# Kernel optimization log

Measured on AMD Instinct MI355X. Metric: run time of the kernel, lower is better.

The kernel has to match this reference:

```python
import jax, jax.numpy as jnp
import numpy as np

CHAINS = [[15, 14, 13], [10, 11, 12], [5, 4, 3], [0, 1, 2]]
B, H, I = 2048, 1024, 3


def setup_inputs() -> dict:
    key = jax.random.key(0)
    ks = jax.random.split(key, 8)
    s = 1.0 / np.sqrt(H)
    return {
        "p3d": jax.random.normal(ks[0], (B, 16, I), dtype=jnp.float32),
        "Wih": jax.random.uniform(ks[1], (4 * H, I), jnp.float32, -s, s),
        "Whh": jax.random.uniform(ks[2], (4 * H, H), jnp.float32, -s, s),
        "bih": jax.random.uniform(ks[3], (4 * H,), jnp.float32, -s, s),
        "bhh": jax.random.uniform(ks[4], (4 * H,), jnp.float32, -s, s),
        "Wref": jax.random.uniform(ks[5], (I, H), jnp.float32, -s, s),
        "bref": jax.random.uniform(ks[6], (I,), jnp.float32, -s, s),
    }


def reference(p3d, Wih, Whh, bih, bhh, Wref, bref):
    # p3d: [B, 16, 3]; shared LSTMCell traverses the skeleton tree fwd+back.
    def cell(x, h, c):
        gates = x @ Wih.T + bih + h @ Whh.T + bhh  # [B, 4H]
        i, f, g, o = jnp.split(gates, 4, axis=-1)  # torch gate order i,f,g,o
        c2 = jax.nn.sigmoid(f) * c + jax.nn.sigmoid(i) * jnp.tanh(g)
        return jax.nn.sigmoid(o) * jnp.tanh(c2), c2

    z = jnp.zeros((p3d.shape[0], Whh.shape[1]), p3d.dtype)
    fh, fc = {}, {}
    # forward pass along limb chains (root of each chain starts from zeros)
    for chain in CHAINS:
        h, c = cell(p3d[:, chain[0]], z, z)
        fh[chain[0]], fc[chain[0]] = h, c
        for prev, cur in zip(chain[:-1], chain[1:]):
            h, c = cell(p3d[:, cur], fh[prev], fc[prev])
            fh[cur], fc[cur] = h, c
    # spine: merge hip ends (joints 2, 3) -> 6 -> 7
    hx, cx = (fh[2] + fh[3]) / 2, (fc[2] + fc[3]) / 2
    fh[6], fc[6] = cell(p3d[:, 6], hx, cx)
    fh[7], fc[7] = cell(p3d[:, 7], fh[6], fc[6])
    # merge neck + wrist ends (joints 7, 13, 12) -> 8 -> 9
    hx = (fh[7] + fh[13] + fh[12]) / 3
    cx = (fc[7] + fc[13] + fc[12]) / 3
    fh[8], fc[8] = cell(p3d[:, 8], hx, cx)
    fh[9], fc[9] = cell(p3d[:, 9], fh[8], fc[8])

    bh, bc = {}, {}
    bh[9], bc[9] = cell(p3d[:, 9], z, z)
    hx, cx = bh[9], bc[9]
    for i in [8, 7, 6]:
        hx, cx = cell(p3d[:, i], hx, cx)
        bh[i], bc[i] = hx, cx
    for chain in CHAINS:
        if chain[2] > 9:
            hx, cx = bh[8], bc[8]
        else:
            hx, cx = bh[6], bc[6]
        for i in reversed(chain):
            hx, cx = cell(p3d[:, i], hx, cx)
            bh[i], bc[i] = hx, cx

    FH = jnp.stack([fh[j] for j in range(16)], axis=1)  # [B, 16, H]
    BH = jnp.stack([bh[j] for j in range(16)], axis=1)  # [B, 16, H]
    out = (FH + BH) / 2.0
    return out @ Wref.T + bref  # [B, 16, 3]
```

## Files before the change

### kernel.cpp

```cpp
#include <hip/hip_runtime.h>
#include <cmath>

#define Bsz 2048
#define Hsz 1024
#define NG  4096
#define BM  128
#define BK  32
#define NKT 32
#define NBUF 3

typedef __attribute__((ext_vector_type(8))) short bf16x8;
typedef __attribute__((ext_vector_type(4))) float f32x4;

struct CellArgs {
  int ncells, b0;
  int joint[8];
  const short* hih[8];
  const short* hil[8];
  const float* cin[8];
  short* hoh[8];
  short* hol[8];
  float* cout[8];
};

struct ProjArgs {
  int ncells, b0;
  int joint[8];
  const short* hh[8];
  const short* hl[8];
};

__device__ __forceinline__ float sigmoidf_(float x) {
  return 1.0f / (1.0f + __expf(-x));
}
__device__ __forceinline__ float fast_tanh(float x) {
  float ax = fabsf(x);
  float e = __expf(2.0f * ax);
  float t = 1.0f - 2.0f / (e + 1.0f);
  return copysignf(t, x);
}
__device__ __forceinline__ float bf2f(short b) {
  unsigned u = ((unsigned)(unsigned short)b) << 16;
  float f; __builtin_memcpy(&f, &u, 4); return f;
}
__device__ __forceinline__ short f2bf(float f) {
  unsigned u; __builtin_memcpy(&u, &f, 4);
  u += 0x7fffu + ((u >> 16) & 1u);
  return (short)(u >> 16);
}
__device__ __forceinline__ void gl_lds16(const void* g, void* l) {
  __builtin_amdgcn_global_load_lds(
      (const __attribute__((address_space(1))) unsigned int*)g,
      (__attribute__((address_space(3))) unsigned int*)l, 16, 0, 0);
}
template <int N> __device__ __forceinline__ void vmw() {
  asm volatile("s_waitcnt vmcnt(%0)" :: "n"(N) : "memory");
}
__device__ __forceinline__ void lgkm0() {
  asm volatile("s_waitcnt lgkmcnt(0)" ::: "memory");
  __builtin_amdgcn_sched_barrier(0);
}

__launch_bounds__(256, 3)
__global__ void cell_kernel(const float* __restrict__ p3d,
                            const short* __restrict__ Whi,
                            const float4* __restrict__ wb,
                            CellArgs A) {
  __shared__ short Atile[NBUF][BM * BK];
  __shared__ short Btile[NBUF][BM * BK];
  __shared__ float xs[BM * 4];

  const int z = blockIdx.z;
  const short* __restrict__ hih = A.hih[z];
  const float* __restrict__ cin = A.cin[z];
  short* __restrict__ hoh = A.hoh[z];
  short* __restrict__ hol = A.hol[z];
  float* __restrict__ co  = A.cout[z];

  const int t = threadIdx.x;
  const int lane = t & 63;
  const int w = t >> 6;
  const int wm = w >> 1;
  const int wn = w & 1;
  const int m0 = blockIdx.x * BM;
  const int hc0 = blockIdx.y * 32;
  const int lc = lane & 15;
  const int kg = lane >> 4;

  const int l2 = lane >> 2;
  const int sslot = ((((lane & 3) - ((lane >> 3) & 3)) & 3) * 8);
  int aOff[2], bOff[2];
  #pragma unroll
  for (int j = 0; j < 2; ++j) {
    const int chunk = j * 4 + w;
    aOff[j] = (m0 + chunk * 16 + l2) * Hsz + sslot;
    const int np = chunk * 16 + l2;
    const int g = np >> 5;
    const int hcl = np & 31;
    bOff[j] = (g * Hsz + hc0 + hcl) * Hsz + sslot;
  }

  if (t < BM) {
    const float* p = p3d + ((size_t)(A.b0 + m0 + t) * 16 + A.joint[z]) * 3;
    xs[t * 4 + 0] = p[0];
    xs[t * 4 + 1] = p[1];
    xs[t * 4 + 2] = p[2];
  }
  __syncthreads();

  f32x4 acc[4][4];
  #pragma unroll
  for (int mf = 0; mf < 4; ++mf)
    #pragma unroll
    for (int nf = 0; nf < 4; ++nf) acc[mf][nf] = (f32x4){0.f, 0.f, 0.f, 0.f};

  const bool hasH = (hih != nullptr);

  auto stage = [&](int kt, int buf) {
    const int k0 = kt * BK;
    #pragma unroll
    for (int j = 0; j < 2; ++j)
      gl_lds16(hih + aOff[j] + k0, &Atile[buf][(j * 4 + w) * 512]);
    #pragma unroll
    for (int j = 0; j < 2; ++j)
      gl_lds16(Whi + bOff[j] + k0, &Btile[buf][(j * 4 + w) * 512]);
  };

  if (hasH) {
    const int rslot = ((kg + (lc >> 1)) & 3) * 8;
    const int aRB = (wm * 64 + lc) * BK + rslot;
    const int bRB = (wn * 16 + lc) * BK + rslot;

    stage(0, 0);
    stage(1, 1);
    vmw<4>();
    __builtin_amdgcn_s_barrier();

    int rb = 0;
    for (int kt = 0; kt < NKT; ++kt) {
      const int sb = (rb + 2 >= NBUF) ? rb + 2 - NBUF : rb + 2;
      if (kt + 2 < NKT) stage(kt + 2, sb);
      const short* Ab = &Atile[rb][0];
      const short* Bb = &Btile[rb][0];
      bf16x8 af[4], bf[4];
      #pragma unroll
      for (int mf = 0; mf < 4; ++mf)
        af[mf] = *(const bf16x8*)(Ab + aRB + mf * 512);
      #pragma unroll
      for (int nf = 0; nf < 4; ++nf)
        bf[nf] = *(const bf16x8*)(Bb + bRB + nf * 1024);
      lgkm0();
      __builtin_amdgcn_s_setprio(1);
      #pragma unroll
      for (int mf = 0; mf < 4; ++mf)
        #pragma unroll
        for (int nf = 0; nf < 4; ++nf)
          acc[mf][nf] = __builtin_amdgcn_mfma_f32_16x16x32_bf16(
              af[mf], bf[nf], acc[mf][nf], 0, 0, 0);
      __builtin_amdgcn_s_setprio(0);
      if (kt + 2 < NKT) vmw<4>();
      else vmw<0>();
      __builtin_amdgcn_s_barrier();
      rb = (rb + 1 >= NBUF) ? 0 : rb + 1;
    }
  }

  const int hc = hc0 + wn * 16 + lc;
  float4 wv[4];
  #pragma unroll
  for (int g = 0; g < 4; ++g) wv[g] = wb[g * Hsz + hc];
  #pragma unroll
  for (int mf = 0; mf < 4; ++mf) {
    #pragma unroll
    for (int r = 0; r < 4; ++r) {
      const int ml = wm * 64 + mf * 16 + kg * 4 + r;
      const int m = m0 + ml;
      const float x0 = xs[ml * 4 + 0], x1 = xs[ml * 4 + 1], x2 = xs[ml * 4 + 2];
      float pre[4];
      #pragma unroll
      for (int g = 0; g < 4; ++g)
        pre[g] = acc[mf][g][r] + wv[g].w + x0 * wv[g].x + x1 * wv[g].y + x2 * wv[g].z;
      const float ci = cin ? cin[(size_t)m * Hsz + hc] : 0.0f;
      const float c2 = sigmoidf_(pre[1]) * ci + sigmoidf_(pre[0]) * fast_tanh(pre[2]);
      const float h2 = sigmoidf_(pre[3]) * fast_tanh(c2);
      co[(size_t)m * Hsz + hc] = c2;
      const short hhi = f2bf(h2);
      hoh[(size_t)m * Hsz + hc] = hhi;
      hol[(size_t)m * Hsz + hc] = f2bf(h2 - bf2f(hhi));
    }
  }
}

__global__ void prep_kernel(const float* __restrict__ Whh,
                            const float* __restrict__ Wih,
                            const float* __restrict__ bih,
                            const float* __restrict__ bhh,
                            short* __restrict__ Whi,
                            float4* __restrict__ wb) {
  const int n4 = NG * Hsz / 4;
  int i = blockIdx.x * blockDim.x + threadIdx.x;
  for (; i < n4; i += gridDim.x * blockDim.x) {
    float4 wv = reinterpret_cast<const float4*>(Whh)[i];
    short4 hi;
    hi.x = f2bf(wv.x);
    hi.y = f2bf(wv.y);
    hi.z = f2bf(wv.z);
    hi.w = f2bf(wv.w);
    reinterpret_cast<short4*>(Whi)[i] = hi;
  }
  int c = blockIdx.x * blockDim.x + threadIdx.x;
  if (c < NG)
    wb[c] = make_float4(Wih[c * 3], Wih[c * 3 + 1], Wih[c * 3 + 2],
                        bih[c] + bhh[c]);
}

__global__ void merge_kernel(short* __restrict__ ohh, short* __restrict__ ohl,
                             float* __restrict__ oc,
                             const short* __restrict__ ahh, const short* __restrict__ ahl,
                             const float* __restrict__ ac,
                             const short* __restrict__ bhh, const short* __restrict__ bhl,
                             const float* __restrict__ bc,
                             const short* __restrict__ chh, const short* __restrict__ chl,
                             const float* __restrict__ cc,
                             float scale, int n4) {
  int i = blockIdx.x * blockDim.x + threadIdx.x;
  for (; i < n4; i += gridDim.x * blockDim.x) {
    short4 ah = reinterpret_cast<const short4*>(ahh)[i];
    short4 al = reinterpret_cast<const short4*>(ahl)[i];
    short4 bh = reinterpret_cast<const short4*>(bhh)[i];
    short4 bl = reinterpret_cast<const short4*>(bhl)[i];
    float h[4];
    h[0] = bf2f(ah.x) + bf2f(al.x) + bf2f(bh.x) + bf2f(bl.x);
    h[1] = bf2f(ah.y) + bf2f(al.y) + bf2f(bh.y) + bf2f(bl.y);
    h[2] = bf2f(ah.z) + bf2f(al.z) + bf2f(bh.z) + bf2f(bl.z);
    h[3] = bf2f(ah.w) + bf2f(al.w) + bf2f(bh.w) + bf2f(bl.w);
    float4 c = reinterpret_cast<const float4*>(ac)[i];
    float4 c2 = reinterpret_cast<const float4*>(bc)[i];
    c.x += c2.x; c.y += c2.y; c.z += c2.z; c.w += c2.w;
    if (chh != nullptr) {
      short4 ch = reinterpret_cast<const short4*>(chh)[i];
      short4 cl = reinterpret_cast<const short4*>(chl)[i];
      h[0] += bf2f(ch.x) + bf2f(cl.x);
      h[1] += bf2f(ch.y) + bf2f(cl.y);
      h[2] += bf2f(ch.z) + bf2f(cl.z);
      h[3] += bf2f(ch.w) + bf2f(cl.w);
      float4 c3 = reinterpret_cast<const float4*>(cc)[i];
      c.x += c3.x; c.y += c3.y; c.z += c3.z; c.w += c3.w;
    }
    short4 hi, lo;
    float v;
    v = h[0] * scale; hi.x = f2bf(v); lo.x = f2bf(v - bf2f(hi.x));
    v = h[1] * scale; hi.y = f2bf(v); lo.y = f2bf(v - bf2f(hi.y));
    v = h[2] * scale; hi.z = f2bf(v); lo.z = f2bf(v - bf2f(hi.z));
    v = h[3] * scale; hi.w = f2bf(v); lo.w = f2bf(v - bf2f(hi.w));
    reinterpret_cast<short4*>(ohh)[i] = hi;
    reinterpret_cast<short4*>(ohl)[i] = lo;
    c.x *= scale; c.y *= scale; c.z *= scale; c.w *= scale;
    reinterpret_cast<float4*>(oc)[i] = c;
  }
}

__global__ void init_out_kernel(float* __restrict__ out, const float* __restrict__ bref) {
  int i = blockIdx.x * blockDim.x + threadIdx.x;
  const int n = Bsz * 16 * 3;
  for (; i < n; i += gridDim.x * blockDim.x) out[i] = bref[i % 3];
}

__global__ void proj_kernel(ProjArgs P, const float* __restrict__ Wref,
                            float* __restrict__ out) {
  const int cell = blockIdx.x;
  const int b = blockIdx.y;
  const int t = threadIdx.x;
  const short4* hh = reinterpret_cast<const short4*>(P.hh[cell] + (size_t)b * Hsz);
  const short4* hl = reinterpret_cast<const short4*>(P.hl[cell] + (size_t)b * Hsz);
  const float4* W0 = reinterpret_cast<const float4*>(Wref);
  const float4* W1 = reinterpret_cast<const float4*>(Wref + Hsz);
  const float4* W2 = reinterpret_cast<const float4*>(Wref + 2 * Hsz);
  short4 a = hh[t], l = hl[t];
  float v0 = 0.5f * (bf2f(a.x) + bf2f(l.x));
  float v1 = 0.5f * (bf2f(a.y) + bf2f(l.y));
  float v2 = 0.5f * (bf2f(a.z) + bf2f(l.z));
  float v3 = 0.5f * (bf2f(a.w) + bf2f(l.w));
  float4 w0 = W0[t], w1 = W1[t], w2 = W2[t];
  float s0 = v0 * w0.x + v1 * w0.y + v2 * w0.z + v3 * w0.w;
  float s1 = v0 * w1.x + v1 * w1.y + v2 * w1.z + v3 * w1.w;
  float s2 = v0 * w2.x + v1 * w2.y + v2 * w2.z + v3 * w2.w;
  #pragma unroll
  for (int off = 32; off > 0; off >>= 1) {
    s0 += __shfl_down(s0, off);
    s1 += __shfl_down(s1, off);
    s2 += __shfl_down(s2, off);
  }
  __shared__ float red[4][3];
  const int wave = t >> 6;
  if ((t & 63) == 0) { red[wave][0] = s0; red[wave][1] = s1; red[wave][2] = s2; }
  __syncthreads();
  if (t == 0) {
    float r0 = red[0][0] + red[1][0] + red[2][0] + red[3][0];
    float r1 = red[0][1] + red[1][1] + red[2][1] + red[3][1];
    float r2 = red[0][2] + red[1][2] + red[2][2] + red[3][2];
    float* o = out + ((size_t)(P.b0 + b) * 16 + P.joint[cell]) * 3;
    atomicAdd(o + 0, r0);
    atomicAdd(o + 1, r1);
    atomicAdd(o + 2, r2);
  }
}

extern "C" void kernel_launch(void* const* d_in, const int* in_sizes, int n_in,
                              void* d_out, int out_size, void* d_ws, size_t ws_size,
                              hipStream_t stream) {
  const float* p3d  = (const float*)d_in[0];
  const float* Wih  = (const float*)d_in[1];
  const float* Whh  = (const float*)d_in[2];
  const float* bih  = (const float*)d_in[3];
  const float* bhh  = (const float*)d_in[4];
  const float* Wref = (const float*)d_in[5];
  const float* bref = (const float*)d_in[6];
  float* out = (float*)d_out;

  char* ws = (char*)d_ws;
  short* Whi = (short*)ws;
  float4* wb = (float4*)(Whi + (size_t)NG * Hsz);
  char* pool = (char*)(wb + NG);
  const size_t fixed = (size_t)(pool - ws);

  int chunkB = Bsz;
  while (chunkB > BM && fixed + (size_t)12 * chunkB * Hsz * 8 > ws_size)
    chunkB >>= 1;
  const size_t CH = (size_t)chunkB * Hsz;
  auto SH = [&](int s) { return (short*)(pool + (size_t)s * CH * 8); };
  auto SL = [&](int s) { return SH(s) + CH; };
  auto SC = [&](int s) { return (float*)(SL(s) + CH); };

  const dim3 blk(256);
  prep_kernel<<<dim3(4096), blk, 0, stream>>>(Whh, Wih, bih, bhh, Whi, wb);
  init_out_kernel<<<dim3(96), blk, 0, stream>>>(out, bref);

  for (int b0 = 0; b0 < Bsz; b0 += chunkB) {
    auto run_cells = [&](CellArgs& A) {
      A.b0 = b0;
      dim3 grid(chunkB / BM, Hsz / 32, A.ncells);
      cell_kernel<<<grid, blk, 0, stream>>>(p3d, Whi, wb, A);
    };
    auto run_proj = [&](ProjArgs& P) {
      P.b0 = b0;
      proj_kernel<<<dim3(P.ncells, chunkB), blk, 0, stream>>>(P, Wref, out);
    };
    auto cellset = [&](CellArgs& A, int i, int joint, int sin, int sout) {
      A.joint[i] = joint;
      if (sin >= 0) { A.hih[i] = SH(sin); A.hil[i] = SL(sin); A.cin[i] = SC(sin); }
      else          { A.hih[i] = nullptr; A.hil[i] = nullptr; A.cin[i] = nullptr; }
      A.hoh[i] = SH(sout); A.hol[i] = SL(sout); A.cout[i] = SC(sout);
    };
    auto projset = [&](ProjArgs& P, int i, int joint, int s) {
      P.joint[i] = joint; P.hh[i] = SH(s); P.hl[i] = SL(s);
    };
    auto domerge = [&](int dst, int s1, int s2, int s3, float scale) {
      merge_kernel<<<dim3(1024), blk, 0, stream>>>(
          SH(dst), SL(dst), SC(dst), SH(s1), SL(s1), SC(s1),
          SH(s2), SL(s2), SC(s2),
          s3 >= 0 ? SH(s3) : nullptr, s3 >= 0 ? SL(s3) : nullptr,
          s3 >= 0 ? SC(s3) : nullptr, scale, (int)(CH / 4));
    };

    {
      CellArgs A{}; A.ncells = 5;
      cellset(A, 0, 15, -1, 0); cellset(A, 1, 10, -1, 1); cellset(A, 2, 5, -1, 2);
      cellset(A, 3,  0, -1, 3); cellset(A, 4,  9, -1, 4);
      run_cells(A);
      ProjArgs P{}; P.ncells = 5;
      projset(P, 0, 15, 0); projset(P, 1, 10, 1); projset(P, 2, 5, 2);
      projset(P, 3,  0, 3); projset(P, 4,  9, 4);
      run_proj(P);
    }
    {
      CellArgs A{}; A.ncells = 5;
      cellset(A, 0, 14, 0, 5); cellset(A, 1, 11, 1, 6); cellset(A, 2, 4, 2, 7);
      cellset(A, 3,  1, 3, 8); cellset(A, 4,  8, 4, 9);
      run_cells(A);
      ProjArgs P{}; P.ncells = 5;
      projset(P, 0, 14, 5); projset(P, 1, 11, 6); projset(P, 2, 4, 7);
      projset(P, 3,  1, 8); projset(P, 4,  8, 9);
      run_proj(P);
    }
    {
      CellArgs A{}; A.ncells = 7;
      cellset(A, 0, 13, 5, 0);  cellset(A, 1, 12, 6, 1);  cellset(A, 2, 3, 7, 2);
      cellset(A, 3,  2, 8, 3);  cellset(A, 4,  7, 9, 4);  cellset(A, 5, 13, 9, 10);
      cellset(A, 6, 12, 9, 11);
      run_cells(A);
      ProjArgs P{}; P.ncells = 7;
      projset(P, 0, 13, 0);  projset(P, 1, 12, 1);  projset(P, 2, 3, 2);
      projset(P, 3,  2, 3);  projset(P, 4,  7, 4);  projset(P, 5, 13, 10);
      projset(P, 6, 12, 11);
      run_proj(P);
    }
    domerge(5, 3, 2, -1, 0.5f);
    {
      CellArgs A{}; A.ncells = 4;
      cellset(A, 0,  6, 5, 6);  cellset(A, 1,  6, 4, 7);
      cellset(A, 2, 14, 10, 8); cellset(A, 3, 11, 11, 9);
      run_cells(A);
      ProjArgs P{}; P.ncells = 4;
      projset(P, 0, 6, 6); projset(P, 1, 6, 7); projset(P, 2, 14, 8);
      projset(P, 3, 11, 9);
      run_proj(P);
    }
    {
      CellArgs A{}; A.ncells = 5;
      cellset(A, 0,  7, 6, 4);  cellset(A, 1, 15, 8, 5);  cellset(A, 2, 10, 9, 10);
      cellset(A, 3,  3, 7, 11); cellset(A, 4,  2, 7, 2);
      run_cells(A);
      ProjArgs P{}; P.ncells = 5;
      projset(P, 0, 7, 4);  projset(P, 1, 15, 5); projset(P, 2, 10, 10);
      projset(P, 3, 3, 11); projset(P, 4,  2, 2);
      run_proj(P);
    }
    domerge(6, 4, 0, 1, 1.0f / 3.0f);
    {
      CellArgs A{}; A.ncells = 3;
      cellset(A, 0, 8, 6, 0); cellset(A, 1, 4, 11, 1); cellset(A, 2, 1, 2, 3);
      run_cells(A);
      ProjArgs P{}; P.ncells = 3;
      projset(P, 0, 8, 0); projset(P, 1, 4, 1); projset(P, 2, 1, 3);
      run_proj(P);
    }
    {
      CellArgs A{}; A.ncells = 3;
      cellset(A, 0, 9, 0, 2); cellset(A, 1, 5, 1, 4); cellset(A, 2, 0, 3, 5);
      run_cells(A);
      ProjArgs P{}; P.ncells = 3;
      projset(P, 0, 9, 2); projset(P, 1, 5, 4); projset(P, 2, 0, 5);
      run_proj(P);
    }
  }
}
```

Measured before the change: 897.4 us.

## Widen cell GEMM tile to 64 hidden columns per block

Each block now computes 64 hidden units (256 gate columns) instead of 32, doubling the B tile and the per-warp MFMA count so each A fragment is reused across twice as many gate columns. The goal is to cut redundant loads of the hidden-state tile and raise the compute-to-load ratio. In exchange, register and LDS use rise, occupancy drops to 2 blocks per CU, and the grid has half as many blocks, which can leave CUs idle.

```diff
diff --git a/kernel.cpp b/kernel.cpp
--- a/kernel.cpp
+++ b/kernel.cpp
@@ -61,13 +61,13 @@
   __builtin_amdgcn_sched_barrier(0);
 }
 
-__launch_bounds__(256, 3)
+__launch_bounds__(256, 2)
 __global__ void cell_kernel(const float* __restrict__ p3d,
                             const short* __restrict__ Whi,
                             const float4* __restrict__ wb,
                             CellArgs A) {
   __shared__ short Atile[NBUF][BM * BK];
-  __shared__ short Btile[NBUF][BM * BK];
+  __shared__ short Btile[NBUF][2 * BM * BK];
   __shared__ float xs[BM * 4];
 
   const int z = blockIdx.z;
@@ -83,21 +83,25 @@
   const int wm = w >> 1;
   const int wn = w & 1;
   const int m0 = blockIdx.x * BM;
-  const int hc0 = blockIdx.y * 32;
+  const int hc0 = blockIdx.y * 64;
   const int lc = lane & 15;
   const int kg = lane >> 4;
 
   const int l2 = lane >> 2;
   const int sslot = ((((lane & 3) - ((lane >> 3) & 3)) & 3) * 8);
-  int aOff[2], bOff[2];
+  int aOff[2], bOff[4];
   #pragma unroll
   for (int j = 0; j < 2; ++j) {
     const int chunk = j * 4 + w;
     aOff[j] = (m0 + chunk * 16 + l2) * Hsz + sslot;
-    const int np = chunk * 16 + l2;
-    const int g = np >> 5;
-    const int hcl = np & 31;
-    bOff[j] = (g * Hsz + hc0 + hcl) * Hsz + sslot;
+  }
+  #pragma unroll
+  for (int j = 0; j < 4; ++j) {
+    const int np = (j * 4 + w) * 16 + l2;
+    const int wq = np >> 7;
+    const int g  = (np >> 5) & 3;
+    const int h5 = np & 31;
+    bOff[j] = (g * Hsz + hc0 + wq * 32 + h5) * Hsz + sslot;
   }
 
   if (t < BM) {
@@ -108,11 +112,11 @@
   }
   __syncthreads();
 
-  f32x4 acc[4][4];
+  f32x4 acc[4][8];
   #pragma unroll
   for (int mf = 0; mf < 4; ++mf)
     #pragma unroll
-    for (int nf = 0; nf < 4; ++nf) acc[mf][nf] = (f32x4){0.f, 0.f, 0.f, 0.f};
+    for (int nf = 0; nf < 8; ++nf) acc[mf][nf] = (f32x4){0.f, 0.f, 0.f, 0.f};
 
   const bool hasH = (hih != nullptr);
 
@@ -122,18 +126,18 @@
     for (int j = 0; j < 2; ++j)
       gl_lds16(hih + aOff[j] + k0, &Atile[buf][(j * 4 + w) * 512]);
     #pragma unroll
-    for (int j = 0; j < 2; ++j)
+    for (int j = 0; j < 4; ++j)
       gl_lds16(Whi + bOff[j] + k0, &Btile[buf][(j * 4 + w) * 512]);
   };
 
   if (hasH) {
     const int rslot = ((kg + (lc >> 1)) & 3) * 8;
     const int aRB = (wm * 64 + lc) * BK + rslot;
-    const int bRB = (wn * 16 + lc) * BK + rslot;
+    const int bRB = (wn * 128 + lc) * BK + rslot;
 
     stage(0, 0);
     stage(1, 1);
-    vmw<4>();
+    vmw<6>();
     __builtin_amdgcn_s_barrier();
 
     int rb = 0;
@@ -142,33 +146,37 @@
       if (kt + 2 < NKT) stage(kt + 2, sb);
       const short* Ab = &Atile[rb][0];
       const short* Bb = &Btile[rb][0];
-      bf16x8 af[4], bf[4];
+      bf16x8 af[4], bf[8];
       #pragma unroll
       for (int mf = 0; mf < 4; ++mf)
         af[mf] = *(const bf16x8*)(Ab + aRB + mf * 512);
       #pragma unroll
-      for (int nf = 0; nf < 4; ++nf)
-        bf[nf] = *(const bf16x8*)(Bb + bRB + nf * 1024);
+      for (int nf = 0; nf < 8; ++nf)
+        bf[nf] = *(const bf16x8*)(Bb + bRB + nf * 512);
       lgkm0();
       __builtin_amdgcn_s_setprio(1);
       #pragma unroll
       for (int mf = 0; mf < 4; ++mf)
         #pragma unroll
-        for (int nf = 0; nf < 4; ++nf)
+        for (int nf = 0; nf < 8; ++nf)
           acc[mf][nf] = __builtin_amdgcn_mfma_f32_16x16x32_bf16(
               af[mf], bf[nf], acc[mf][nf], 0, 0, 0);
       __builtin_amdgcn_s_setprio(0);
-      if (kt + 2 < NKT) vmw<4>();
+      if (kt + 2 < NKT) vmw<6>();
       else vmw<0>();
       __builtin_amdgcn_s_barrier();
       rb = (rb + 1 >= NBUF) ? 0 : rb + 1;
     }
   }
 
-  const int hc = hc0 + wn * 16 + lc;
-  float4 wv[4];
-  #pragma unroll
-  for (int g = 0; g < 4; ++g) wv[g] = wb[g * Hsz + hc];
+  float4 wv[2][4];
+  int hcl[2];
+  #pragma unroll
+  for (int hcp = 0; hcp < 2; ++hcp) {
+    hcl[hcp] = hc0 + wn * 32 + hcp * 16 + lc;
+    #pragma unroll
+    for (int g = 0; g < 4; ++g) wv[hcp][g] = wb[g * Hsz + hcl[hcp]];
+  }
   #pragma unroll
   for (int mf = 0; mf < 4; ++mf) {
     #pragma unroll
@@ -176,17 +184,22 @@
       const int ml = wm * 64 + mf * 16 + kg * 4 + r;
       const int m = m0 + ml;
       const float x0 = xs[ml * 4 + 0], x1 = xs[ml * 4 + 1], x2 = xs[ml * 4 + 2];
-      float pre[4];
       #pragma unroll
-      for (int g = 0; g < 4; ++g)
-        pre[g] = acc[mf][g][r] + wv[g].w + x0 * wv[g].x + x1 * wv[g].y + x2 * wv[g].z;
-      const float ci = cin ? cin[(size_t)m * Hsz + hc] : 0.0f;
-      const float c2 = sigmoidf_(pre[1]) * ci + sigmoidf_(pre[0]) * fast_tanh(pre[2]);
-      const float h2 = sigmoidf_(pre[3]) * fast_tanh(c2);
-      co[(size_t)m * Hsz + hc] = c2;
-      const short hhi = f2bf(h2);
-      hoh[(size_t)m * Hsz + hc] = hhi;
-      hol[(size_t)m * Hsz + hc] = f2bf(h2 - bf2f(hhi));
+      for (int hcp = 0; hcp < 2; ++hcp) {
+        const int hc = hcl[hcp];
+        float pre[4];
+        #pragma unroll
+        for (int g = 0; g < 4; ++g)
+          pre[g] = acc[mf][g * 2 + hcp][r] + wv[hcp][g].w +
+                   x0 * wv[hcp][g].x + x1 * wv[hcp][g].y + x2 * wv[hcp][g].z;
+        const float ci = cin ? cin[(size_t)m * Hsz + hc] : 0.0f;
+        const float c2 = sigmoidf_(pre[1]) * ci + sigmoidf_(pre[0]) * fast_tanh(pre[2]);
+        const float h2 = sigmoidf_(pre[3]) * fast_tanh(c2);
+        co[(size_t)m * Hsz + hc] = c2;
+        const short hhi = f2bf(h2);
+        hoh[(size_t)m * Hsz + hc] = hhi;
+        hol[(size_t)m * Hsz + hc] = f2bf(h2 - bf2f(hhi));
+      }
     }
   }
 }
@@ -339,7 +352,7 @@
   for (int b0 = 0; b0 < Bsz; b0 += chunkB) {
     auto run_cells = [&](CellArgs& A) {
       A.b0 = b0;
-      dim3 grid(chunkB / BM, Hsz / 32, A.ncells);
+      dim3 grid(chunkB / BM, Hsz / 64, A.ncells);
       cell_kernel<<<grid, blk, 0, stream>>>(p3d, Whi, wb, A);
     };
     auto run_proj = [&](ProjArgs& P) {
```

Result: no change. 902.6 us (+0.6%).

## Deepen LDS prefetch with register double-buffered fragments and skip dead cell-state stores

Applied to the files above, without the earlier changes.

Restructures the recurrent GEMM main loop to prefetch three K tiles into the triple LDS buffer and to double-buffer MFMA operand fragments in registers. Each step now loads the next tile's fragments from LDS while the current MFMAs run. This is meant to hide LDS read latency behind matrix math, at the cost of more vector registers and a possible occupancy drop. Separately, cells whose c output is never read (leaf cells of the backward pass) now skip the float cell-state store, reducing global write traffic.

```diff
diff --git a/kernel.cpp b/kernel.cpp
--- a/kernel.cpp
+++ b/kernel.cpp
@@ -133,35 +133,68 @@
 
     stage(0, 0);
     stage(1, 1);
-    vmw<4>();
+    stage(2, 2);
+    vmw<6>();
     __builtin_amdgcn_s_barrier();
 
+    bf16x8 fa0[4], fb0[4], fa1[4], fb1[4];
+    #pragma unroll
+    for (int i = 0; i < 4; ++i) {
+      fa0[i] = *(const bf16x8*)(&Atile[0][0] + aRB + i * 512);
+      fb0[i] = *(const bf16x8*)(&Btile[0][0] + bRB + i * 1024);
+    }
+
     int rb = 0;
-    for (int kt = 0; kt < NKT; ++kt) {
-      const int sb = (rb + 2 >= NBUF) ? rb + 2 - NBUF : rb + 2;
-      if (kt + 2 < NKT) stage(kt + 2, sb);
-      const short* Ab = &Atile[rb][0];
-      const short* Bb = &Btile[rb][0];
-      bf16x8 af[4], bf[4];
-      #pragma unroll
-      for (int mf = 0; mf < 4; ++mf)
-        af[mf] = *(const bf16x8*)(Ab + aRB + mf * 512);
-      #pragma unroll
-      for (int nf = 0; nf < 4; ++nf)
-        bf[nf] = *(const bf16x8*)(Bb + bRB + nf * 1024);
-      lgkm0();
-      __builtin_amdgcn_s_setprio(1);
-      #pragma unroll
-      for (int mf = 0; mf < 4; ++mf)
+    for (int kt = 0; kt < NKT; kt += 2) {
+      {
+        const int rn = (rb + 1 >= NBUF) ? 0 : rb + 1;
+        if (kt + 1 < NKT) {
+          #pragma unroll
+          for (int i = 0; i < 4; ++i) {
+            fa1[i] = *(const bf16x8*)(&Atile[rn][0] + aRB + i * 512);
+            fb1[i] = *(const bf16x8*)(&Btile[rn][0] + bRB + i * 1024);
+          }
+        }
+        if (kt + 3 < NKT) stage(kt + 3, rb);
+        __builtin_amdgcn_s_setprio(1);
         #pragma unroll
-        for (int nf = 0; nf < 4; ++nf)
-          acc[mf][nf] = __builtin_amdgcn_mfma_f32_16x16x32_bf16(
-              af[mf], bf[nf], acc[mf][nf], 0, 0, 0);
-      __builtin_amdgcn_s_setprio(0);
-      if (kt + 2 < NKT) vmw<4>();
-      else vmw<0>();
-      __builtin_amdgcn_s_barrier();
-      rb = (rb + 1 >= NBUF) ? 0 : rb + 1;
+        for (int mf = 0; mf < 4; ++mf)
+          #pragma unroll
+          for (int nf = 0; nf < 4; ++nf)
+            acc[mf][nf] = __builtin_amdgcn_mfma_f32_16x16x32_bf16(
+                fa0[mf], fb0[nf], acc[mf][nf], 0, 0, 0);
+        __builtin_amdgcn_s_setprio(0);
+        lgkm0();
+        if (kt + 3 < NKT) vmw<6>();
+        else vmw<0>();
+        __builtin_amdgcn_s_barrier();
+        rb = rn;
+      }
+      {
+        const int ko = kt + 1;
+        const int rn = (rb + 1 >= NBUF) ? 0 : rb + 1;
+        if (ko + 1 < NKT) {
+          #pragma unroll
+          for (int i = 0; i < 4; ++i) {
+            fa0[i] = *(const bf16x8*)(&Atile[rn][0] + aRB + i * 512);
+            fb0[i] = *(const bf16x8*)(&Btile[rn][0] + bRB + i * 1024);
+          }
+        }
+        if (ko + 3 < NKT) stage(ko + 3, rb);
+        __builtin_amdgcn_s_setprio(1);
+        #pragma unroll
+        for (int mf = 0; mf < 4; ++mf)
+          #pragma unroll
+          for (int nf = 0; nf < 4; ++nf)
+            acc[mf][nf] = __builtin_amdgcn_mfma_f32_16x16x32_bf16(
+                fa1[mf], fb1[nf], acc[mf][nf], 0, 0, 0);
+        __builtin_amdgcn_s_setprio(0);
+        lgkm0();
+        if (ko + 3 < NKT) vmw<6>();
+        else vmw<0>();
+        __builtin_amdgcn_s_barrier();
+        rb = rn;
+      }
     }
   }
 
@@ -183,7 +216,7 @@
       const float ci = cin ? cin[(size_t)m * Hsz + hc] : 0.0f;
       const float c2 = sigmoidf_(pre[1]) * ci + sigmoidf_(pre[0]) * fast_tanh(pre[2]);
       const float h2 = sigmoidf_(pre[3]) * fast_tanh(c2);
-      co[(size_t)m * Hsz + hc] = c2;
+      if (co) co[(size_t)m * Hsz + hc] = c2;
       const short hhi = f2bf(h2);
       hoh[(size_t)m * Hsz + hc] = hhi;
       hol[(size_t)m * Hsz + hc] = f2bf(h2 - bf2f(hhi));
@@ -346,11 +379,13 @@
       P.b0 = b0;
       proj_kernel<<<dim3(P.ncells, chunkB), blk, 0, stream>>>(P, Wref, out);
     };
-    auto cellset = [&](CellArgs& A, int i, int joint, int sin, int sout) {
+    auto cellset = [&](CellArgs& A, int i, int joint, int sin, int sout,
+                       bool cstore = true) {
       A.joint[i] = joint;
       if (sin >= 0) { A.hih[i] = SH(sin); A.hil[i] = SL(sin); A.cin[i] = SC(sin); }
       else          { A.hih[i] = nullptr; A.hil[i] = nullptr; A.cin[i] = nullptr; }
-      A.hoh[i] = SH(sout); A.hol[i] = SL(sout); A.cout[i] = SC(sout);
+      A.hoh[i] = SH(sout); A.hol[i] = SL(sout);
+      A.cout[i] = cstore ? SC(sout) : nullptr;
     };
     auto projset = [&](ProjArgs& P, int i, int joint, int s) {
       P.joint[i] = joint; P.hh[i] = SH(s); P.hl[i] = SL(s);
@@ -408,8 +443,9 @@
     }
     {
       CellArgs A{}; A.ncells = 5;
-      cellset(A, 0,  7, 6, 4);  cellset(A, 1, 15, 8, 5);  cellset(A, 2, 10, 9, 10);
-      cellset(A, 3,  3, 7, 11); cellset(A, 4,  2, 7, 2);
+      cellset(A, 0,  7, 6, 4);         cellset(A, 1, 15, 8, 5, false);
+      cellset(A, 2, 10, 9, 10, false); cellset(A, 3,  3, 7, 11);
+      cellset(A, 4,  2, 7, 2);
       run_cells(A);
       ProjArgs P{}; P.ncells = 5;
       projset(P, 0, 7, 4);  projset(P, 1, 15, 5); projset(P, 2, 10, 10);
@@ -427,7 +463,8 @@
     }
     {
       CellArgs A{}; A.ncells = 3;
-      cellset(A, 0, 9, 0, 2); cellset(A, 1, 5, 1, 4); cellset(A, 2, 0, 3, 5);
+      cellset(A, 0, 9, 0, 2, false); cellset(A, 1, 5, 1, 4, false);
+      cellset(A, 2, 0, 3, 5, false);
       run_cells(A);
       ProjArgs P{}; P.ncells = 3;
       projset(P, 0, 9, 2); projset(P, 1, 5, 4); projset(P, 2, 0, 5);
```

After: 894.9 us. Within noise of the previous version (-0.3%).
